# Kernel optimization log

Measured on AMD Instinct MI355X. Metric: run time of the kernel, lower is better.

The kernel has to match this reference:

```python
import jax, jax.numpy as jnp
import numpy as np

# Unpooled output spatial size (pooled 128x128 -> unpooled 256x256)
OUT_H, OUT_W = 256, 256


def setup_inputs() -> dict:
    key = jax.random.key(0)
    k1, k2, k3, k4 = jax.random.split(key, 4)
    B, C, OH, OW = 16, 64, 128, 128
    K, P = 4, 4  # kernel_size samples, bilinear taps
    x = jax.random.normal(k1, (B, C, OH, OW), dtype=jnp.float32)
    idx_mask = jax.random.randint(k2, (B, C, OH, OW), 0, K, dtype=jnp.int64)
    sample_map = jax.random.randint(k3, (OH, OW, K, P), 0, OUT_H * OUT_W, dtype=jnp.int64)
    interp_weights = jax.random.uniform(k4, (OH, OW, K, P), dtype=jnp.float32)
    return {"x": x, "idx_mask": idx_mask, "sample_map": sample_map,
            "interp_weights": interp_weights}


def reference(x, idx_mask, sample_map, interp_weights):
    # x: (B,C,OH,OW) pooled values; idx_mask: (B,C,OH,OW) argmax kernel sample in [0,K)
    # sample_map: (OH,OW,K,P) flat indices into OUT_H*OUT_W; interp_weights: (OH,OW,K,P)
    B, C, OH, OW = x.shape
    P = sample_map.shape[-1]
    oh = jnp.arange(OH)[:, None]
    ow = jnp.arange(OW)[None, :]
    # Select, per (b,c,oh,ow), the winning kernel sample's taps and weights -> (B,C,OH,OW,P)
    sel_idx = sample_map[oh, ow, idx_mask]
    sel_w = interp_weights[oh, ow, idx_mask]
    vals = sel_w * x[..., None]  # (B,C,OH,OW,P)
    bb = jnp.arange(B)[:, None, None, None, None]
    cc = jnp.arange(C)[None, :, None, None, None]
    out = jnp.zeros((B, C, OUT_H * OUT_W), dtype=x.dtype)
    out = out.at[bb, cc, sel_idx].add(vals)  # scatter-add (atomic add in CUDA kernel)
    return out.reshape(B, C, OUT_H, OUT_W)
```

## Files before the change

### kernel.cpp

```cpp
#include <hip/hip_runtime.h>
#include <hip/hip_fp16.h>

constexpr int B  = 16;
constexpr int C  = 64;
constexpr int OH = 128;
constexpr int OW = 128;
constexpr int HW = OH * OW;
constexpr int K  = 4;
constexpr int P  = 4;
constexpr int TAPS = HW * K * P;
constexpr int OUT_H = 256;
constexpr int OUT_W = 256;
constexpr int PLANE = OUT_H * OUT_W;
constexpr int NQ = 4;
constexpr int QUARTER = PLANE / NQ;
constexpr int BLOCK = 512;
constexpr size_t TABLE_BYTES = (size_t)HW * K * 16;

constexpr int GW = 4;
constexpr int NGROUP = PLANE / 64;

constexpr int E2CAP = 229376;
constexpr size_t WS_V2_BYTES = ((size_t)PLANE * 4 + 2048) * 4 + (size_t)E2CAP * 16;

constexpr int CHUNK_CAP = 114688;
constexpr size_t WS_SORT_BYTES = ((size_t)PLANE * 5) * 4 + (size_t)CHUNK_CAP * 16;

static __device__ __forceinline__ float h2f(unsigned short u) {
    __half h; __builtin_memcpy(&h, &u, 2); return __half2float(h);
}


__global__ __launch_bounds__(256) void hist_kernel(
    const int* __restrict__ sm, unsigned* __restrict__ counts)
{
    int r = blockIdx.x * 256 + threadIdx.x;
    if (r < TAPS) atomicAdd(&counts[sm[r]], 1u);
}


__global__ __launch_bounds__(256) void zero_v2_kernel(
    unsigned* __restrict__ counts, unsigned* __restrict__ cursor,
    uint4* __restrict__ entries2)
{
    int r = blockIdx.x * 256 + threadIdx.x;
    if (r < PLANE) { counts[r] = 0u; cursor[r] = 0u; }
    if (r < E2CAP) entries2[r] = make_uint4(0u, 0u, 0u, 0u);
}

constexpr int WNB = 32;
__global__ __launch_bounds__(256) void window_sort_v2_kernel(
    const unsigned* __restrict__ counts, unsigned* __restrict__ sched)
{
    __shared__ unsigned hist[WNB];
    __shared__ unsigned cur[WNB];
    const int w = blockIdx.x;
    const int t = threadIdx.x;
    const int base = w * 1024;
    if (t < WNB) hist[t] = 0;
    __syncthreads();
    unsigned nch[4];
    for (int j = 0; j < 4; ++j) {
        unsigned c = counts[base + t * 4 + j];
        nch[j] = (c + 3u) >> 2; if (nch[j] > 31u) nch[j] = 31u;
        atomicAdd(&hist[nch[j]], 1u);
    }
    __syncthreads();
    if (t == 0) {
        unsigned run = 0;
        for (int b = 0; b < WNB; ++b) { unsigned v = hist[b]; cur[b] = run; run += v; }
    }
    __syncthreads();
    for (int j = 0; j < 4; ++j) {
        unsigned p = atomicAdd(&cur[nch[j]], 1u);
        sched[base + p] = (unsigned)(base + t * 4 + j);
    }
}

__global__ __launch_bounds__(1024) void group_scan_kernel(
    const unsigned* __restrict__ counts, const unsigned* __restrict__ sched,
    unsigned* __restrict__ gdesc, unsigned* __restrict__ wbase)
{
    __shared__ unsigned part[NGROUP];
    const int g = threadIdx.x;
    unsigned olast = sched[g * 64 + 63];
    unsigned M = (counts[olast] + 3u) >> 2;
    part[g] = M;
    __syncthreads();
    for (int st = 1; st < NGROUP; st <<= 1) {
        unsigned v = (g >= st) ? part[g - st] : 0u;
        __syncthreads();
        part[g] += v;
        __syncthreads();
    }
    unsigned rowbase = part[g] - M;
    gdesc[g] = (rowbase << 6) | (M << 24);
    unsigned wb = (rowbase << 6) * 4u;
    for (int l = 0; l < 64; ++l)
        wbase[sched[g * 64 + l]] = wb + (unsigned)(l * 4);
}

__global__ __launch_bounds__(256) void scatter_v2_kernel(
    const int* __restrict__ sm, const float* __restrict__ iw,
    unsigned* __restrict__ cursor, const unsigned* __restrict__ wbase,
    unsigned* __restrict__ entries2_u32)
{
    int r = blockIdx.x * 256 + threadIdx.x;
    if (r >= TAPS) return;
    int o = sm[r];
    unsigned hw = (unsigned)(r >> 4);
    unsigned k  = (unsigned)((r >> 2) & 3);
    __half h = __float2half_rn(iw[r]);
    unsigned short hb; __builtin_memcpy(&hb, &h, 2);
    unsigned ent = (hw << 2) | k | ((unsigned)hb << 16);
    unsigned idx = atomicAdd(&cursor[o], 1u);
    entries2_u32[wbase[o] + ((idx >> 2) << 8) + (idx & 3u)] = ent;
}

__global__ __launch_bounds__(1024) void unpool_grouped_kernel(
    const float* __restrict__ x,
    const int*   __restrict__ idx_mask,
    const unsigned* __restrict__ sched,
    const unsigned* __restrict__ gdesc,
    const uint4* __restrict__ entries2,
    float* __restrict__ out)
{
    __shared__ unsigned xk[HW];
    __shared__ float    stg[GW * 1024];

    const int bc = blockIdx.x;
    const float4* xp4 = (const float4*)(x + (size_t)bc * HW);
    const int4*   ip4 = (const int4*)(idx_mask + (size_t)bc * HW);
    uint4* xk4 = (uint4*)xk;

    for (int t = threadIdx.x; t < HW / 4; t += 1024) {
        float4 xv = xp4[t];
        int4   kv = ip4[t];
        uint4 o;
        o.x = (__float_as_uint(xv.x) & ~3u) | ((unsigned)kv.x & 3u);
        o.y = (__float_as_uint(xv.y) & ~3u) | ((unsigned)kv.y & 3u);
        o.z = (__float_as_uint(xv.z) & ~3u) | ((unsigned)kv.z & 3u);
        o.w = (__float_as_uint(xv.w) & ~3u) | ((unsigned)kv.w & 3u);
        xk4[t] = o;
    }
    __syncthreads();

    const char* xkb = (const char*)xk;
    const float4* stg4 = (const float4*)stg;
    float4* op4 = (float4*)(out + (size_t)bc * PLANE);

    const int lane = threadIdx.x & 63;
    const int wid  = threadIdx.x >> 6;

#define PROC1(E) { unsigned e = (E); \
    unsigned u = *(const unsigned*)(xkb + (e & 0xfffcu)); \
    float w = (((u ^ e) & 3u) == 0u) ? h2f((unsigned short)(e >> 16)) : 0.f; \
    acc = fmaf(w, __uint_as_float(u), acc); }

    for (int gq = 0; gq < PLANE / 1024 / GW; ++gq) {
        for (int iw2 = 0; iw2 < GW; ++iw2) {
            const int i = gq * GW + iw2;
            const int s = (wid + i) & 15;
            const int g = i * 16 + s;
            const unsigned gd = gdesc[g];
            const unsigned M  = gd >> 24;
            const uint4* ep = entries2 + (gd & 0xffffffu) + lane;
            float acc = 0.f;
            if (M) {
                uint4 ch = ep[0];
                for (unsigned j = 1; j < M; ++j) {
                    uint4 nx = ep[j << 6];
                    PROC1(ch.x) PROC1(ch.y) PROC1(ch.z) PROC1(ch.w)
                    ch = nx;
                }
                PROC1(ch.x) PROC1(ch.y) PROC1(ch.z) PROC1(ch.w)
            }
            const unsigned oid = sched[g * 64 + lane];
            stg[iw2 * 1024 + (oid & 1023u)] = acc;
        }
        __syncthreads();
        op4[gq * 1024 + threadIdx.x] = stg4[threadIdx.x];
        __syncthreads();
    }
#undef PROC1
}


__global__ __launch_bounds__(256) void zero_ws_kernel(
    unsigned* __restrict__ counts, uint4* __restrict__ entries)
{
    int r = blockIdx.x * 256 + threadIdx.x;
    if (r < PLANE)     counts[r]  = 0u;
    if (r < CHUNK_CAP) entries[r] = make_uint4(0u, 0u, 0u, 0u);
}

__global__ __launch_bounds__(1024) void scan_chunks_kernel(
    const unsigned* __restrict__ counts,
    unsigned* __restrict__ desc, unsigned* __restrict__ cursor)
{
    __shared__ unsigned part[1024];
    const int t = threadIdx.x;
    const int base = t * 64;
    unsigned s = 0;
    for (int j = 0; j < 64; ++j) s += (counts[base + j] + 3u) >> 2;
    part[t] = s;
    __syncthreads();
    for (int st = 1; st < 1024; st <<= 1) {
        unsigned v = (t >= st) ? part[t - st] : 0u;
        __syncthreads();
        part[t] += v;
        __syncthreads();
    }
    unsigned run = part[t] - s;
    for (int j = 0; j < 64; ++j) {
        unsigned c   = counts[base + j];
        unsigned nch = (c + 3u) >> 2;
        desc[base + j]   = run | (nch << 24);
        cursor[base + j] = run * 4u;
        run += nch;
    }
}

__global__ __launch_bounds__(256) void scatter_chunks_kernel(
    const int* __restrict__ sm, const float* __restrict__ iw,
    unsigned* __restrict__ cursor, unsigned* __restrict__ entries_u32)
{
    int r = blockIdx.x * 256 + threadIdx.x;
    if (r >= TAPS) return;
    int o = sm[r];
    unsigned hw = (unsigned)(r >> 4);
    unsigned k  = (unsigned)((r >> 2) & 3);
    __half h = __float2half_rn(iw[r]);
    unsigned short hb; __builtin_memcpy(&hb, &h, 2);
    unsigned ent = (hw << 2) | k | ((unsigned)hb << 16);
    unsigned pos = atomicAdd(&cursor[o], 1u);
    entries_u32[pos] = ent;
}

__global__ __launch_bounds__(256) void window_sort_kernel(
    const unsigned* __restrict__ desc, uint2* __restrict__ sched)
{
    __shared__ unsigned hist[WNB];
    __shared__ unsigned cur[WNB];
    const int w = blockIdx.x;
    const int t = threadIdx.x;
    const int base = w * 1024;
    if (t < WNB) hist[t] = 0;
    __syncthreads();
    unsigned d[4], nch[4];
    for (int j = 0; j < 4; ++j) {
        d[j] = desc[base + t * 4 + j];
        nch[j] = d[j] >> 24; if (nch[j] > 31u) nch[j] = 31u;
        atomicAdd(&hist[nch[j]], 1u);
    }
    __syncthreads();
    if (t == 0) {
        unsigned run = 0;
        for (int b = 0; b < WNB; ++b) { unsigned v = hist[b]; cur[b] = run; run += v; }
    }
    __syncthreads();
    for (int j = 0; j < 4; ++j) {
        unsigned p = atomicAdd(&cur[nch[j]], 1u);
        sched[base + p] = make_uint2(d[j], (unsigned)(base + t * 4 + j));
    }
}

__global__ __launch_bounds__(1024) void unpool_staged_kernel(
    const float* __restrict__ x,
    const int*   __restrict__ idx_mask,
    const uint2* __restrict__ sched,
    const uint4* __restrict__ entries,
    float* __restrict__ out)
{
    __shared__ unsigned xk[HW];
    __shared__ float    stg[GW * 1024];

    const int bc = blockIdx.x;
    const float4* xp4 = (const float4*)(x + (size_t)bc * HW);
    const int4*   ip4 = (const int4*)(idx_mask + (size_t)bc * HW);
    uint4* xk4 = (uint4*)xk;

    for (int t = threadIdx.x; t < HW / 4; t += 1024) {
        float4 xv = xp4[t];
        int4   kv = ip4[t];
        uint4 o;
        o.x = (__float_as_uint(xv.x) & ~3u) | ((unsigned)kv.x & 3u);
        o.y = (__float_as_uint(xv.y) & ~3u) | ((unsigned)kv.y & 3u);
        o.z = (__float_as_uint(xv.z) & ~3u) | ((unsigned)kv.z & 3u);
        o.w = (__float_as_uint(xv.w) & ~3u) | ((unsigned)kv.w & 3u);
        xk4[t] = o;
    }
    __syncthreads();

    const char* xkb = (const char*)xk;
    const float4* stg4 = (const float4*)stg;
    float4* op4 = (float4*)(out + (size_t)bc * PLANE);

    const int lane = threadIdx.x & 63;
    const int wid  = threadIdx.x >> 6;

    for (int g = 0; g < PLANE / 1024 / GW; ++g) {
        for (int iw2 = 0; iw2 < GW; ++iw2) {
            const int i = g * GW + iw2;
            const int slot = i * 1024 + (((wid + i) & 15) << 6) + lane;
            const uint2 s = sched[slot];
            const unsigned nch = s.x >> 24;
            const uint4* ep = entries + (s.x & 0xffffffu);
            float acc = 0.f;
            for (unsigned j = 0; j < nch; ++j) {
                uint4 ch = ep[j];
                {   unsigned e = ch.x;
                    unsigned u = *(const unsigned*)(xkb + (e & 0xfffcu));
                    float w = (((u ^ e) & 3u) == 0u) ? h2f((unsigned short)(e >> 16)) : 0.f;
                    acc = fmaf(w, __uint_as_float(u & ~3u), acc); }
                {   unsigned e = ch.y;
                    unsigned u = *(const unsigned*)(xkb + (e & 0xfffcu));
                    float w = (((u ^ e) & 3u) == 0u) ? h2f((unsigned short)(e >> 16)) : 0.f;
                    acc = fmaf(w, __uint_as_float(u & ~3u), acc); }
                {   unsigned e = ch.z;
                    unsigned u = *(const unsigned*)(xkb + (e & 0xfffcu));
                    float w = (((u ^ e) & 3u) == 0u) ? h2f((unsigned short)(e >> 16)) : 0.f;
                    acc = fmaf(w, __uint_as_float(u & ~3u), acc); }
                {   unsigned e = ch.w;
                    unsigned u = *(const unsigned*)(xkb + (e & 0xfffcu));
                    float w = (((u ^ e) & 3u) == 0u) ? h2f((unsigned short)(e >> 16)) : 0.f;
                    acc = fmaf(w, __uint_as_float(u & ~3u), acc); }
            }
            stg[iw2 * 1024 + (s.y & 1023)] = acc;
        }
        __syncthreads();
        op4[g * 1024 + threadIdx.x] = stg4[threadIdx.x];
        __syncthreads();
    }
}


static __device__ __forceinline__ uint4 sel4(bool c, uint4 a, uint4 b) {
    return make_uint4(c ? a.x : b.x, c ? a.y : b.y, c ? a.z : b.z, c ? a.w : b.w);
}
static __device__ __forceinline__ float2 u2f2(unsigned u) {
    __half2 h; __builtin_memcpy(&h, &u, 4); return __half22float2(h);
}

__global__ __launch_bounds__(256) void compact_table_kernel(
    const int4* __restrict__ sm, const float4* __restrict__ iw, uint4* __restrict__ ct)
{
    int r = blockIdx.x * blockDim.x + threadIdx.x;
    if (r >= HW * K) return;
    int4   s = sm[r];
    float4 w = iw[r];
    uint4 o;
    o.x = ((unsigned)s.x & 0xffffu) | (((unsigned)s.y & 0xffffu) << 16);
    o.y = ((unsigned)s.z & 0xffffu) | (((unsigned)s.w & 0xffffu) << 16);
    __half2 h01 = __floats2half2_rn(w.x, w.y);
    __half2 h23 = __floats2half2_rn(w.z, w.w);
    __builtin_memcpy(&o.z, &h01, 4);
    __builtin_memcpy(&o.w, &h23, 4);
    ct[r] = o;
}

__global__ __launch_bounds__(BLOCK) void unpool_lds2_kernel(
    const float* __restrict__ x,
    const int*   __restrict__ idx_mask,
    const uint4* __restrict__ ct,
    float* __restrict__ out)
{
    __shared__ float acc[QUARTER];

    const int bc    = blockIdx.x >> 2;
    const int q     = blockIdx.x & 3;
    const int qbase = q * QUARTER;

    float4* acc4 = (float4*)acc;
    for (int t = threadIdx.x; t < QUARTER / 4; t += BLOCK)
        acc4[t] = make_float4(0.f, 0.f, 0.f, 0.f);
    __syncthreads();

    const float* xp = x + (size_t)bc * HW;
    const int*   ip = idx_mask + (size_t)bc * HW;

    for (int hw = threadIdx.x; hw < HW; hw += BLOCK) {
        float xv = xp[hw];
        int   k  = ip[hw];
        const uint4* c = ct + (hw << 2);
        uint4 r0 = c[0], r1 = c[1], r2 = c[2], r3 = c[3];
        uint4 rl = sel4(k & 1, r1, r0);
        uint4 rh = sel4(k & 1, r3, r2);
        uint4 r  = sel4(k & 2, rh, rl);

        int i0 = r.x & 0xffff, i1 = (int)(r.x >> 16);
        int i2 = r.y & 0xffff, i3 = (int)(r.y >> 16);
        float2 w01 = u2f2(r.z);
        float2 w23 = u2f2(r.w);

        int a;
        a = i0 - qbase; if ((unsigned)a < (unsigned)QUARTER) atomicAdd(&acc[a], w01.x * xv);
        a = i1 - qbase; if ((unsigned)a < (unsigned)QUARTER) atomicAdd(&acc[a], w01.y * xv);
        a = i2 - qbase; if ((unsigned)a < (unsigned)QUARTER) atomicAdd(&acc[a], w23.x * xv);
        a = i3 - qbase; if ((unsigned)a < (unsigned)QUARTER) atomicAdd(&acc[a], w23.y * xv);
    }
    __syncthreads();

    float4* op4 = (float4*)(out + (size_t)bc * PLANE + qbase);
    for (int t = threadIdx.x; t < QUARTER / 4; t += BLOCK)
        op4[t] = acc4[t];
}

__global__ __launch_bounds__(256) void unpool_lds_fallback_kernel(
    const float* __restrict__ x,
    const int*   __restrict__ idx_mask,
    const int4*  __restrict__ sample_map,
    const float4* __restrict__ interp_w,
    float* __restrict__ out)
{
    __shared__ float acc[QUARTER];
    const int bc    = blockIdx.x >> 2;
    const int q     = blockIdx.x & 3;
    const int qbase = q * QUARTER;
    float4* acc4 = (float4*)acc;
    for (int t = threadIdx.x; t < QUARTER / 4; t += 256)
        acc4[t] = make_float4(0.f, 0.f, 0.f, 0.f);
    __syncthreads();
    const float* xp = x + (size_t)bc * HW;
    const int*   ip = idx_mask + (size_t)bc * HW;
    for (int hw = threadIdx.x; hw < HW; hw += 256) {
        float xv = xp[hw];
        int   k  = ip[hw];
        int row = hw * K + k;
        int4   sel = sample_map[row];
        float4 w   = interp_w[row];
        int a;
        a = sel.x - qbase; if ((unsigned)a < (unsigned)QUARTER) atomicAdd(&acc[a], w.x * xv);
        a = sel.y - qbase; if ((unsigned)a < (unsigned)QUARTER) atomicAdd(&acc[a], w.y * xv);
        a = sel.z - qbase; if ((unsigned)a < (unsigned)QUARTER) atomicAdd(&acc[a], w.z * xv);
        a = sel.w - qbase; if ((unsigned)a < (unsigned)QUARTER) atomicAdd(&acc[a], w.w * xv);
    }
    __syncthreads();
    float4* op4 = (float4*)(out + (size_t)bc * PLANE + qbase);
    for (int t = threadIdx.x; t < QUARTER / 4; t += 256)
        op4[t] = acc4[t];
}

extern "C" void kernel_launch(void* const* d_in, const int* in_sizes, int n_in,
                              void* d_out, int out_size, void* d_ws, size_t ws_size,
                              hipStream_t stream) {
    const float*  x          = (const float*)d_in[0];
    const int*    idx_mask   = (const int*)d_in[1];
    const int*    sample_map = (const int*)d_in[2];
    const float*  interp_w   = (const float*)d_in[3];
    float* out = (float*)d_out;

    if (ws_size >= WS_V2_BYTES) {
        unsigned* counts   = (unsigned*)d_ws;
        unsigned* cursor   = counts + PLANE;
        unsigned* sched    = cursor + PLANE;
        unsigned* wbase    = sched + PLANE;
        unsigned* gdesc    = wbase + PLANE;
        uint4*    entries2 = (uint4*)(gdesc + 2048);

        zero_v2_kernel<<<(E2CAP + 255) / 256, 256, 0, stream>>>(counts, cursor, entries2);
        hist_kernel<<<TAPS / 256, 256, 0, stream>>>(sample_map, counts);
        window_sort_v2_kernel<<<PLANE / 1024, 256, 0, stream>>>(counts, sched);
        group_scan_kernel<<<1, NGROUP, 0, stream>>>(counts, sched, gdesc, wbase);
        scatter_v2_kernel<<<TAPS / 256, 256, 0, stream>>>(
            sample_map, interp_w, cursor, wbase, (unsigned*)entries2);
        unpool_grouped_kernel<<<B * C, 1024, 0, stream>>>(
            x, idx_mask, sched, gdesc, entries2, out);
    } else if (ws_size >= WS_SORT_BYTES) {
        unsigned* desc    = (unsigned*)d_ws;
        unsigned* cursor  = desc + PLANE;
        unsigned* counts  = cursor + PLANE;
        uint2*    sched   = (uint2*)(counts + PLANE);
        uint4*    entries = (uint4*)(counts + PLANE + 2 * PLANE);

        zero_ws_kernel<<<(CHUNK_CAP + 255) / 256, 256, 0, stream>>>(counts, entries);
        hist_kernel<<<TAPS / 256, 256, 0, stream>>>(sample_map, counts);
        scan_chunks_kernel<<<1, 1024, 0, stream>>>(counts, desc, cursor);
        scatter_chunks_kernel<<<TAPS / 256, 256, 0, stream>>>(
            sample_map, interp_w, cursor, (unsigned*)entries);
        window_sort_kernel<<<PLANE / 1024, 256, 0, stream>>>(desc, sched);
        unpool_staged_kernel<<<B * C, 1024, 0, stream>>>(x, idx_mask, sched, entries, out);
    } else if (ws_size >= TABLE_BYTES) {
        uint4* ct = (uint4*)d_ws;
        compact_table_kernel<<<(HW * K + 255) / 256, 256, 0, stream>>>(
            (const int4*)sample_map, (const float4*)interp_w, ct);
        unpool_lds2_kernel<<<B * C * NQ, BLOCK, 0, stream>>>(
            x, idx_mask, ct, out);
    } else {
        unpool_lds_fallback_kernel<<<B * C * NQ, 256, 0, stream>>>(
            x, idx_mask, (const int4*)sample_map, (const float4*)interp_w, out);
    }
}
```

Baseline: 541.2 us.

## Use per-k fp16 shared-memory x table with packed fdot2 and parallelize wbase

The unpool kernel now stores x in shared memory as fp16, expanded into four slots per pooled pixel. Only the slot matching idx_mask holds the value and the others are zero, so the per-tap mask compare and select disappear. Pairs of taps are then combined with a perm and a packed fp16 dot2 instruction into an fp32 accumulator. Separately, the serial per-group wbase write loop moves out of the single-block scan into its own fully parallel kernel. The trade-offs are that shared memory per block roughly doubles, which lowers occupancy, and that x loses precision by being rounded to fp16.

New measurement: 630.4 us. 16.5% more time.

```diff
diff --git a/kernel.cpp b/kernel.cpp
--- a/kernel.cpp
+++ b/kernel.cpp
@@ -30,6 +30,11 @@
     __half h; __builtin_memcpy(&h, &u, 2); return __half2float(h);
 }
 
+typedef _Float16 h2_t __attribute__((ext_vector_type(2)));
+static __device__ __forceinline__ h2_t as_h2(unsigned u) {
+    h2_t r; __builtin_memcpy(&r, &u, 4); return r;
+}
+
 
 __global__ __launch_bounds__(256) void hist_kernel(
     const int* __restrict__ sm, unsigned* __restrict__ counts)
@@ -77,14 +82,13 @@
     }
 }
 
-__global__ __launch_bounds__(1024) void group_scan_kernel(
+__global__ __launch_bounds__(1024) void scan_m_kernel(
     const unsigned* __restrict__ counts, const unsigned* __restrict__ sched,
-    unsigned* __restrict__ gdesc, unsigned* __restrict__ wbase)
+    unsigned* __restrict__ gdesc)
 {
     __shared__ unsigned part[NGROUP];
     const int g = threadIdx.x;
-    unsigned olast = sched[g * 64 + 63];
-    unsigned M = (counts[olast] + 3u) >> 2;
+    unsigned M = (counts[sched[g * 64 + 63]] + 3u) >> 2;
     part[g] = M;
     __syncthreads();
     for (int st = 1; st < NGROUP; st <<= 1) {
@@ -95,9 +99,16 @@
     }
     unsigned rowbase = part[g] - M;
     gdesc[g] = (rowbase << 6) | (M << 24);
-    unsigned wb = (rowbase << 6) * 4u;
-    for (int l = 0; l < 64; ++l)
-        wbase[sched[g * 64 + l]] = wb + (unsigned)(l * 4);
+}
+
+__global__ __launch_bounds__(1024) void wbase_kernel(
+    const unsigned* __restrict__ sched, const unsigned* __restrict__ gdesc,
+    unsigned* __restrict__ wbase)
+{
+    const int slot = blockIdx.x * 1024 + threadIdx.x;
+    const unsigned o = sched[slot];
+    const unsigned g = (unsigned)slot >> 6, l = (unsigned)slot & 63u;
+    wbase[o] = ((gdesc[g] & 0xffffffu) + l) * 4u;
 }
 
 __global__ __launch_bounds__(256) void scatter_v2_kernel(
@@ -117,7 +128,7 @@
     entries2_u32[wbase[o] + ((idx >> 2) << 8) + (idx & 3u)] = ent;
 }
 
-__global__ __launch_bounds__(1024) void unpool_grouped_kernel(
+__global__ __launch_bounds__(1024) void unpool_dot_kernel(
     const float* __restrict__ x,
     const int*   __restrict__ idx_mask,
     const unsigned* __restrict__ sched,
@@ -125,37 +136,53 @@
     const uint4* __restrict__ entries2,
     float* __restrict__ out)
 {
-    __shared__ unsigned xk[HW];
-    __shared__ float    stg[GW * 1024];
+    __shared__ unsigned short xkh[HW * 4];
+    __shared__ float stg[GW * 1024];
 
     const int bc = blockIdx.x;
     const float4* xp4 = (const float4*)(x + (size_t)bc * HW);
     const int4*   ip4 = (const int4*)(idx_mask + (size_t)bc * HW);
-    uint4* xk4 = (uint4*)xk;
+    uint2* xk2 = (uint2*)xkh;
 
     for (int t = threadIdx.x; t < HW / 4; t += 1024) {
         float4 xv = xp4[t];
         int4   kv = ip4[t];
-        uint4 o;
-        o.x = (__float_as_uint(xv.x) & ~3u) | ((unsigned)kv.x & 3u);
-        o.y = (__float_as_uint(xv.y) & ~3u) | ((unsigned)kv.y & 3u);
-        o.z = (__float_as_uint(xv.z) & ~3u) | ((unsigned)kv.z & 3u);
-        o.w = (__float_as_uint(xv.w) & ~3u) | ((unsigned)kv.w & 3u);
-        xk4[t] = o;
-    }
-    __syncthreads();
-
-    const char* xkb = (const char*)xk;
+        float xs[4] = {xv.x, xv.y, xv.z, xv.w};
+        int   ks[4] = {kv.x, kv.y, kv.z, kv.w};
+        for (int c = 0; c < 4; ++c) {
+            __half h = __float2half_rn(xs[c]);
+            unsigned short hb; __builtin_memcpy(&hb, &h, 2);
+            unsigned k = (unsigned)ks[c] & 3u;
+            unsigned sh = ((unsigned)hb) << ((k & 1u) << 4);
+            uint2 v;
+            v.x = (k & 2u) ? 0u : sh;
+            v.y = (k & 2u) ? sh : 0u;
+            xk2[t * 4 + c] = v;
+        }
+    }
+    __syncthreads();
+
+    const char* xkb = (const char*)xkh;
     const float4* stg4 = (const float4*)stg;
     float4* op4 = (float4*)(out + (size_t)bc * PLANE);
 
     const int lane = threadIdx.x & 63;
     const int wid  = threadIdx.x >> 6;
 
-#define PROC1(E) { unsigned e = (E); \
-    unsigned u = *(const unsigned*)(xkb + (e & 0xfffcu)); \
-    float w = (((u ^ e) & 3u) == 0u) ? h2f((unsigned short)(e >> 16)) : 0.f; \
-    acc = fmaf(w, __uint_as_float(u), acc); }
+#if __has_builtin(__builtin_amdgcn_perm) && __has_builtin(__builtin_amdgcn_fdot2)
+#define PAIR(Ea, Eb) { \
+    unsigned ua = *(const unsigned short*)(xkb + (((Ea) & 0xffffu) << 1)); \
+    unsigned ub = *(const unsigned short*)(xkb + (((Eb) & 0xffffu) << 1)); \
+    unsigned xp_ = __builtin_amdgcn_perm(ub, ua, 0x05040100u); \
+    unsigned wp_ = __builtin_amdgcn_perm((Eb), (Ea), 0x07060302u); \
+    acc = __builtin_amdgcn_fdot2(as_h2(xp_), as_h2(wp_), acc, false); }
+#else
+#define PAIR(Ea, Eb) { \
+    unsigned ua = *(const unsigned short*)(xkb + (((Ea) & 0xffffu) << 1)); \
+    unsigned ub = *(const unsigned short*)(xkb + (((Eb) & 0xffffu) << 1)); \
+    acc = fmaf(h2f((unsigned short)((Ea) >> 16)), h2f((unsigned short)ua), acc); \
+    acc = fmaf(h2f((unsigned short)((Eb) >> 16)), h2f((unsigned short)ub), acc); }
+#endif
 
     for (int gq = 0; gq < PLANE / 1024 / GW; ++gq) {
         for (int iw2 = 0; iw2 < GW; ++iw2) {
@@ -170,10 +197,10 @@
                 uint4 ch = ep[0];
                 for (unsigned j = 1; j < M; ++j) {
                     uint4 nx = ep[j << 6];
-                    PROC1(ch.x) PROC1(ch.y) PROC1(ch.z) PROC1(ch.w)
+                    PAIR(ch.x, ch.y) PAIR(ch.z, ch.w)
                     ch = nx;
                 }
-                PROC1(ch.x) PROC1(ch.y) PROC1(ch.z) PROC1(ch.w)
+                PAIR(ch.x, ch.y) PAIR(ch.z, ch.w)
             }
             const unsigned oid = sched[g * 64 + lane];
             stg[iw2 * 1024 + (oid & 1023u)] = acc;
@@ -182,7 +209,7 @@
         op4[gq * 1024 + threadIdx.x] = stg4[threadIdx.x];
         __syncthreads();
     }
-#undef PROC1
+#undef PAIR
 }
 
 
@@ -441,6 +468,24 @@
         op4[t] = acc4[t];
 }
 
+static void launch_r7_pipeline(const float* x, const int* idx_mask,
+                               const int* sample_map, const float* interp_w,
+                               float* out, void* d_ws, hipStream_t stream) {
+    unsigned* desc    = (unsigned*)d_ws;
+    unsigned* cursor  = desc + PLANE;
+    unsigned* counts  = cursor + PLANE;
+    uint2*    sched   = (uint2*)(counts + PLANE);
+    uint4*    entries = (uint4*)(counts + PLANE + 2 * PLANE);
+
+    zero_ws_kernel<<<(CHUNK_CAP + 255) / 256, 256, 0, stream>>>(counts, entries);
+    hist_kernel<<<TAPS / 256, 256, 0, stream>>>(sample_map, counts);
+    scan_chunks_kernel<<<1, 1024, 0, stream>>>(counts, desc, cursor);
+    scatter_chunks_kernel<<<TAPS / 256, 256, 0, stream>>>(
+        sample_map, interp_w, cursor, (unsigned*)entries);
+    window_sort_kernel<<<PLANE / 1024, 256, 0, stream>>>(desc, sched);
+    unpool_staged_kernel<<<B * C, 1024, 0, stream>>>(x, idx_mask, sched, entries, out);
+}
+
 extern "C" void kernel_launch(void* const* d_in, const int* in_sizes, int n_in,
                               void* d_out, int out_size, void* d_ws, size_t ws_size,
                               hipStream_t stream) {
@@ -461,25 +506,17 @@
         zero_v2_kernel<<<(E2CAP + 255) / 256, 256, 0, stream>>>(counts, cursor, entries2);
         hist_kernel<<<TAPS / 256, 256, 0, stream>>>(sample_map, counts);
         window_sort_v2_kernel<<<PLANE / 1024, 256, 0, stream>>>(counts, sched);
-        group_scan_kernel<<<1, NGROUP, 0, stream>>>(counts, sched, gdesc, wbase);
+        scan_m_kernel<<<1, NGROUP, 0, stream>>>(counts, sched, gdesc);
+        wbase_kernel<<<PLANE / 1024, 1024, 0, stream>>>(sched, gdesc, wbase);
         scatter_v2_kernel<<<TAPS / 256, 256, 0, stream>>>(
             sample_map, interp_w, cursor, wbase, (unsigned*)entries2);
-        unpool_grouped_kernel<<<B * C, 1024, 0, stream>>>(
+        unpool_dot_kernel<<<B * C, 1024, 0, stream>>>(
             x, idx_mask, sched, gdesc, entries2, out);
+        if (hipGetLastError() != hipSuccess) {
+            launch_r7_pipeline(x, idx_mask, sample_map, interp_w, out, d_ws, stream);
+        }
     } else if (ws_size >= WS_SORT_BYTES) {
-        unsigned* desc    = (unsigned*)d_ws;
-        unsigned* cursor  = desc + PLANE;
-        unsigned* counts  = cursor + PLANE;
-        uint2*    sched   = (uint2*)(counts + PLANE);
-        uint4*    entries = (uint4*)(counts + PLANE + 2 * PLANE);
-
-        zero_ws_kernel<<<(CHUNK_CAP + 255) / 256, 256, 0, stream>>>(counts, entries);
-        hist_kernel<<<TAPS / 256, 256, 0, stream>>>(sample_map, counts);
-        scan_chunks_kernel<<<1, 1024, 0, stream>>>(counts, desc, cursor);
-        scatter_chunks_kernel<<<TAPS / 256, 256, 0, stream>>>(
-            sample_map, interp_w, cursor, (unsigned*)entries);
-        window_sort_kernel<<<PLANE / 1024, 256, 0, stream>>>(desc, sched);
-        unpool_staged_kernel<<<B * C, 1024, 0, stream>>>(x, idx_mask, sched, entries, out);
+        launch_r7_pipeline(x, idx_mask, sample_map, interp_w, out, d_ws, stream);
     } else if (ws_size >= TABLE_BYTES) {
         uint4* ct = (uint4*)d_ws;
         compact_table_kernel<<<(HW * K + 255) / 256, 256, 0, stream>>>(
```
